# Kernel tuning notes

Measured on AMD Instinct MI355X. Metric: run time of the kernel, lower is better.

## Reference

```python
import jax, jax.numpy as jnp
import numpy as np

B, S, D, H = 4, 2048, 512, 8
EPS = 1e-5

def _layer_norm(x, gamma, beta):
    mu = jnp.mean(x, axis=-1, keepdims=True)
    var = jnp.mean(jnp.square(x - mu), axis=-1, keepdims=True)
    return (x - mu) * jax.lax.rsqrt(var + EPS) * gamma + beta

def setup_inputs() -> dict:
    key = jax.random.key(0)
    ks = jax.random.split(key, 6)
    sc = 1.0 / np.sqrt(D)
    return {
        "seq_k": jax.random.normal(ks[0], (B, S, D), jnp.float32),
        "seq_q": jax.random.normal(ks[1], (B, S, D), jnp.float32),
        "seq_v": jax.random.normal(ks[2], (B, S, D), jnp.float32),
        "W1": jax.random.normal(ks[3], (D, D), jnp.float32) * sc,
        "W2": jax.random.normal(ks[4], (D, D), jnp.float32) * sc,
        "W3": jax.random.normal(ks[5], (D, D), jnp.float32) * sc,
        "gamma": jnp.ones((D,), jnp.float32),
        "beta": jnp.zeros((D,), jnp.float32),
    }

def reference(seq_k, seq_q, seq_v, W1, W2, W3, gamma, beta):
    # is_layer_norm=True: pre-LN on values; seq_v_value is the normed v
    v_in = _layer_norm(seq_v, gamma, beta)
    # nn.Linear(bias=False): y = x @ W^T
    q = seq_q @ W1.T
    k = seq_k @ W2.T
    v = v_in @ W3.T
    hd = D // H
    q = q.reshape(B, S, H, hd).transpose(0, 2, 1, 3)  # b h s d
    k = k.reshape(B, S, H, hd).transpose(0, 2, 1, 3)
    v = v.reshape(B, S, H, hd).transpose(0, 2, 1, 3)
    # faithful quirk: scores = K @ Q^T, unscaled
    scores = jnp.einsum("bhid,bhjd->bhij", k, q)  # b h s s
    attn = jax.nn.softmax(scores, axis=-1)
    out = jnp.einsum("bhij,bhjd->bhid", attn, v)  # b h s d
    out = out.transpose(0, 2, 1, 3).reshape(B, S, D)
    out = out + v_in                 # is_residual=True
    return _layer_norm(out, gamma, beta)  # final LN
```

## Files before the change

kernel.cpp:

```cpp
#include <hip/hip_runtime.h>
#include <math.h>

#define BB 4
#define SS 2048
#define DD 512
#define HH 8
#define HD 64
#define NTOK (BB*SS)
#define EPS 1e-5f
#define NE ((size_t)NTOK * DD)
#define WN ((size_t)DD * DD)
#define LOG2E 1.4426950408889634f

typedef _Float16 half8v __attribute__((ext_vector_type(8)));
typedef _Float16 half4v __attribute__((ext_vector_type(4)));
typedef _Float16 half2v __attribute__((ext_vector_type(2)));
typedef float f32x4 __attribute__((ext_vector_type(4)));

__device__ __forceinline__ float fast_exp2(float x) {
#if __has_builtin(__builtin_amdgcn_exp2f)
    return __builtin_amdgcn_exp2f(x);
#else
    return __expf(x * 0.6931471805599453f);
#endif
}

__device__ __forceinline__ half2v pack2(float a, float b) {
    return __builtin_bit_cast(half2v, __builtin_amdgcn_cvt_pkrtz(a, b));
}

__device__ __forceinline__ half4v pack4(float a, float b, float c, float d) {
    half2v lo = pack2(a, b);
    half2v hi = pack2(c, d);
    half4v r; r[0] = lo[0]; r[1] = lo[1]; r[2] = hi[0]; r[3] = hi[1];
    return r;
}

__device__ __forceinline__ void gload_lds16(const void* g, void* l) {
    __builtin_amdgcn_global_load_lds(
        (const __attribute__((address_space(1))) unsigned int*)g,
        (__attribute__((address_space(3))) unsigned int*)l, 16, 0, 0);
}

__global__ __launch_bounds__(256) void ln_kernel(const _Float16* __restrict__ x,
                                                 const _Float16* __restrict__ res,
                                                 const float* __restrict__ gamma,
                                                 const float* __restrict__ beta,
                                                 float* __restrict__ y) {
    int row = blockIdx.x;
    int t = threadIdx.x;
    half2v xv = *(const half2v*)&x[(size_t)row * DD + 2 * t];
    half2v rv = *(const half2v*)&res[(size_t)row * DD + 2 * t];
    float2 v;
    v.x = (float)xv[0] + (float)rv[0];
    v.y = (float)xv[1] + (float)rv[1];
    float s = v.x + v.y;
    float ss = v.x * v.x + v.y * v.y;
    #pragma unroll
    for (int off = 32; off; off >>= 1) {
        s  += __shfl_down(s,  off);
        ss += __shfl_down(ss, off);
    }
    __shared__ float ws0[4], ws1[4];
    int wid = t >> 6, lane = t & 63;
    if (lane == 0) { ws0[wid] = s; ws1[wid] = ss; }
    __syncthreads();
    __shared__ float mu_s, rstd_s;
    if (t == 0) {
        float S0 = ws0[0] + ws0[1] + ws0[2] + ws0[3];
        float S1 = ws1[0] + ws1[1] + ws1[2] + ws1[3];
        float mu = S0 * (1.0f / DD);
        float var = S1 * (1.0f / DD) - mu * mu;
        mu_s = mu;
        rstd_s = rsqrtf(var + EPS);
    }
    __syncthreads();
    float mu = mu_s, rstd = rstd_s;
    float2 g = ((const float2*)gamma)[t];
    float2 bb = ((const float2*)beta)[t];
    float2 o;
    o.x = (v.x - mu) * rstd * g.x + bb.x;
    o.y = (v.y - mu) * rstd * g.y + bb.y;
    ((float2*)(y + (size_t)row * DD))[t] = o;
}

__global__ __launch_bounds__(256) void prep_kernel(const float* __restrict__ seq_v,
                                                   const float* __restrict__ seq_q,
                                                   const float* __restrict__ seq_k,
                                                   const float* __restrict__ W1,
                                                   const float* __restrict__ W2,
                                                   const float* __restrict__ W3,
                                                   const float* __restrict__ gamma,
                                                   const float* __restrict__ beta,
                                                   _Float16* __restrict__ v16,
                                                   _Float16* __restrict__ qk16,
                                                   _Float16* __restrict__ w16) {
    int bid = blockIdx.x;
    int t = threadIdx.x;
    if (bid < NTOK) {
        int row = bid;
        float2 v = ((const float2*)(seq_v + (size_t)row * DD))[t];
        float s = v.x + v.y;
        float ss = v.x * v.x + v.y * v.y;
        #pragma unroll
        for (int off = 32; off; off >>= 1) {
            s  += __shfl_down(s,  off);
            ss += __shfl_down(ss, off);
        }
        __shared__ float ws0[4], ws1[4];
        int wid = t >> 6, lane = t & 63;
        if (lane == 0) { ws0[wid] = s; ws1[wid] = ss; }
        __syncthreads();
        __shared__ float mu_s, rstd_s;
        if (t == 0) {
            float S0 = ws0[0] + ws0[1] + ws0[2] + ws0[3];
            float S1 = ws1[0] + ws1[1] + ws1[2] + ws1[3];
            float mu = S0 * (1.0f / DD);
            float var = S1 * (1.0f / DD) - mu * mu;
            mu_s = mu;
            rstd_s = rsqrtf(var + EPS);
        }
        __syncthreads();
        float mu = mu_s, rstd = rstd_s;
        float2 g = ((const float2*)gamma)[t];
        float2 bb = ((const float2*)beta)[t];
        float2 o;
        o.x = (v.x - mu) * rstd * g.x + bb.x;
        o.y = (v.y - mu) * rstd * g.y + bb.y;
        *(half2v*)&v16[(size_t)row * DD + 2 * t] = pack2(o.x, o.y);
    } else if (bid < 2 * NTOK) {
        size_t i = ((size_t)(bid - NTOK) * 256 + t) * 4;
        const float* src = (i < NE) ? (seq_q + i) : (seq_k + (i - NE));
        float4 v = *(const float4*)src;
        *(half4v*)(qk16 + i) = pack4(v.x, v.y, v.z, v.w);
    } else {
        size_t i = ((size_t)(bid - 2 * NTOK) * 256 + t) * 4;
        const float* src; float sc;
        if (i < WN)          { src = W1 + i;            sc = LOG2E; }
        else if (i < 2 * WN) { src = W2 + (i - WN);     sc = 1.0f; }
        else                 { src = W3 + (i - 2 * WN); sc = 1.0f; }
        float4 v = *(const float4*)src;
        *(half4v*)(w16 + i) = pack4(v.x * sc, v.y * sc, v.z * sc, v.w * sc);
    }
}

#define GBM 128
#define GBN 128
#define GBK 64
__global__ __launch_bounds__(256) void gemm_mfma(const _Float16* __restrict__ Aall,
                                                 const _Float16* __restrict__ Wall,
                                                 _Float16* __restrict__ Call,
                                                 _Float16* __restrict__ vtOut) {
    __shared__ __align__(16) _Float16 smem[2][2 * GBM * GBK];
    int wg = blockIdx.x;
    int local = wg >> 3;
    int z = local >> 5;
    int r5 = local & 31;
    int my = (wg & 7) * 8 + (r5 >> 2);
    int nx = r5 & 3;
    bool isv = (z == 2);
    const _Float16* A = Aall + (size_t)z * NE;
    const _Float16* W = Wall + (size_t)z * WN;
    int t = threadIdx.x, w = t >> 6, lane = t & 63, q = lane >> 4, ln = lane & 15;
    int lrow = lane >> 3, lseg = lane & 7;
    int m0 = my * GBM, n0 = nx * GBN;
    int wm = w & 1, wn = w >> 1;
    f32x4 acc[4][4];
    #pragma unroll
    for (int mt = 0; mt < 4; ++mt)
        #pragma unroll
        for (int nt = 0; nt < 4; ++nt)
            acc[mt][nt] = (f32x4){0.f, 0.f, 0.f, 0.f};

    int gs = lseg ^ lrow;

    auto stage = [&](int k0, int buf) {
        _Float16* Asb = smem[buf];
        _Float16* Wsb = smem[buf] + GBM * GBK;
        #pragma unroll
        for (int p = 0; p < 4; ++p) {
            int rr = w * 32 + p * 8 + lrow;
            gload_lds16(A + (size_t)(m0 + rr) * DD + k0 + gs * 8,
                        Asb + (size_t)(w * 32 + p * 8) * GBK);
            gload_lds16(W + (size_t)(n0 + rr) * DD + k0 + gs * 8,
                        Wsb + (size_t)(w * 32 + p * 8) * GBK);
        }
    };

    stage(0, 0);
    const int NK = DD / GBK;
    for (int ki = 0; ki < NK; ++ki) {
        int cur = ki & 1;
        __syncthreads();
        if (ki + 1 < NK) stage((ki + 1) * GBK, cur ^ 1);
        _Float16* Asb = smem[cur];
        _Float16* Wsb = smem[cur] + GBM * GBK;
        __builtin_amdgcn_s_setprio(1);
        #pragma unroll
        for (int kk = 0; kk < 2; ++kk) {
            int ch = ((4 * kk + q) ^ (ln & 7)) * 8;
            half8v af[4], wf[4];
            #pragma unroll
            for (int mt = 0; mt < 4; ++mt)
                af[mt] = *(half8v*)&Asb[(wm * 64 + mt * 16 + ln) * GBK + ch];
            #pragma unroll
            for (int nt = 0; nt < 4; ++nt)
                wf[nt] = *(half8v*)&Wsb[(wn * 64 + nt * 16 + ln) * GBK + ch];
            if (!isv) {
                #pragma unroll
                for (int mt = 0; mt < 4; ++mt)
                    #pragma unroll
                    for (int nt = 0; nt < 4; ++nt)
                        acc[mt][nt] = __builtin_amdgcn_mfma_f32_16x16x32_f16(
                            wf[nt], af[mt], acc[mt][nt], 0, 0, 0);
            } else {
                #pragma unroll
                for (int mt = 0; mt < 4; ++mt)
                    #pragma unroll
                    for (int nt = 0; nt < 4; ++nt)
                        acc[mt][nt] = __builtin_amdgcn_mfma_f32_16x16x32_f16(
                            af[mt], wf[nt], acc[mt][nt], 0, 0, 0);
            }
        }
        __builtin_amdgcn_s_setprio(0);
    }

    _Float16* esm = &smem[0][0];
    if (!isv) {
        #pragma unroll
        for (int mt = 0; mt < 4; ++mt) {
            int mloc = wm * 64 + mt * 16 + ln;
            #pragma unroll
            for (int nt = 0; nt < 4; ++nt) {
                int nloc = wn * 64 + nt * 16 + q * 4;
                int cs = (nloc >> 3) ^ (mloc & 7);
                char* p = (char*)esm + mloc * 256 + cs * 16 + (nloc & 7) * 2;
                *(half4v*)p = pack4(acc[mt][nt][0], acc[mt][nt][1],
                                    acc[mt][nt][2], acc[mt][nt][3]);
            }
        }
    } else {
        #pragma unroll
        for (int nt = 0; nt < 4; ++nt) {
            int dloc = wn * 64 + nt * 16 + ln;
            #pragma unroll
            for (int mt = 0; mt < 4; ++mt) {
                int sloc = wm * 64 + mt * 16 + q * 4;
                int cs = (sloc >> 3) ^ (dloc & 7);
                char* p = (char*)esm + dloc * 256 + cs * 16 + (sloc & 7) * 2;
                *(half4v*)p = pack4(acc[mt][nt][0], acc[mt][nt][1],
                                    acc[mt][nt][2], acc[mt][nt][3]);
            }
        }
    }
    __syncthreads();
    int bq = m0 >> 11, sbase = m0 & (SS - 1);
    if (!isv) {
        _Float16* C = Call + (size_t)z * NE;
        #pragma unroll
        for (int p = 0; p < 8; ++p) {
            int id = p * 256 + t;
            int rr = id >> 4, c = id & 15;
            half8v vv = *(half8v*)((char*)esm + rr * 256 + ((c ^ (rr & 7)) * 16));
            int n = n0 + c * 8;
            int h = n >> 6, d0 = n & 63;
            *(half8v*)&C[((size_t)(bq * HH + h) * SS + (sbase + rr)) * HD + d0] = vv;
        }
    } else {
        #pragma unroll
        for (int p = 0; p < 8; ++p) {
            int id = p * 256 + t;
            int rr = id >> 4, c = id & 15;
            half8v vv = *(half8v*)((char*)esm + rr * 256 + ((c ^ (rr & 7)) * 16));
            int d = n0 + rr;
            int h = d >> 6, dd = d & 63;
            *(half8v*)&vtOut[((size_t)(bq * HH + h) * HD + dd) * SS + sbase + c * 8] = vv;
        }
    }
}

#define AI 128
#define AJ 64
__global__ __launch_bounds__(512, 4) void attn_mfma(const _Float16* __restrict__ qh,
                                                    const _Float16* __restrict__ kh,
                                                    const _Float16* __restrict__ vt,
                                                    _Float16* __restrict__ outp) {
    __shared__ __align__(16) _Float16 Qt[2][AJ * HD];
    __shared__ __align__(16) _Float16 Vs[2][HD * AJ];
    __shared__ __align__(16) _Float16 Ps[AI * AJ];
    int t = threadIdx.x, w = t >> 6, lane = t & 63, q = lane >> 4, ln = lane & 15;
    int wg = blockIdx.x;
    int slot = wg >> 3;
    int bh = (wg & 7) * 4 + (slot >> 4);
    int i0 = (slot & 15) * AI;
    int b = bh >> 3, h = bh & 7;
    const _Float16* Kb = kh + (size_t)bh * SS * HD;
    const _Float16* Qb = qh + (size_t)bh * SS * HD;
    const _Float16* Vb = vt + (size_t)bh * HD * SS;

    half8v kf[2];
    #pragma unroll
    for (int kk = 0; kk < 2; ++kk)
        kf[kk] = *(const half8v*)&Kb[(size_t)(i0 + w * 16 + ln) * HD + kk * 32 + q * 8];

    f32x4 oacc[4], lacc;
    float m_run = -3.0e38f;
    lacc = (f32x4){0.f, 0.f, 0.f, 0.f};
    #pragma unroll
    for (int mtd = 0; mtd < 4; ++mtd) oacc[mtd] = (f32x4){0.f, 0.f, 0.f, 0.f};
    half8v ones;
    #pragma unroll
    for (int e = 0; e < 8; ++e) ones[e] = (_Float16)1.0f;
    const f32x4 zf = (f32x4){0.f, 0.f, 0.f, 0.f};

    int sr = t >> 3;
    int sc = t & 7;
    int ssw = sc ^ (sr & 7);

    gload_lds16(Qb + (size_t)sr * HD + ssw * 8, &Qt[0][(size_t)w * 512]);
    gload_lds16(Vb + (size_t)sr * SS + ssw * 8, &Vs[0][(size_t)w * 512]);

    const int NITER = SS / AJ;

#define ATTN_STEP(JT, CUR, DOPF)                                              \
    {                                                                         \
        __syncthreads();                                                      \
        if (DOPF) {                                                           \
            int j1 = ((JT) + 1) * AJ;                                         \
            gload_lds16(Qb + (size_t)(j1 + sr) * HD + ssw * 8,                \
                        &Qt[(CUR) ^ 1][(size_t)w * 512]);                     \
            gload_lds16(Vb + (size_t)sr * SS + j1 + ssw * 8,                  \
                        &Vs[(CUR) ^ 1][(size_t)w * 512]);                     \
        }                                                                     \
        f32x4 sacc[4];                                                        \
        __builtin_amdgcn_s_setprio(1);                                        \
        _Pragma("unroll")                                                     \
        for (int mt = 0; mt < 4; ++mt) {                                      \
            half8v qf = *(half8v*)&Qt[CUR][(mt * 16 + ln) * HD +              \
                                           (q ^ (ln & 7)) * 8];               \
            sacc[mt] = __builtin_amdgcn_mfma_f32_16x16x32_f16(                \
                qf, kf[0], zf, 0, 0, 0);                                      \
        }                                                                     \
        _Pragma("unroll")                                                     \
        for (int mt = 0; mt < 4; ++mt) {                                      \
            half8v qf = *(half8v*)&Qt[CUR][(mt * 16 + ln) * HD +              \
                                           ((4 + q) ^ (ln & 7)) * 8];         \
            sacc[mt] = __builtin_amdgcn_mfma_f32_16x16x32_f16(                \
                qf, kf[1], sacc[mt], 0, 0, 0);                                \
        }                                                                     \
        __builtin_amdgcn_s_setprio(0);                                        \
        float mx = fmaxf(fmaxf(sacc[0][0], sacc[0][1]),                       \
                         fmaxf(sacc[0][2], sacc[0][3]));                      \
        _Pragma("unroll")                                                     \
        for (int mt = 1; mt < 4; ++mt) {                                      \
            float m2 = fmaxf(fmaxf(sacc[mt][0], sacc[mt][1]),                 \
                             fmaxf(sacc[mt][2], sacc[mt][3]));                \
            mx = fmaxf(mx, m2);                                               \
        }                                                                     \
        mx = fmaxf(mx, __shfl_xor(mx, 16));                                   \
        mx = fmaxf(mx, __shfl_xor(mx, 32));                                   \
        if (__any(mx > m_run + 7.0f)) {                                       \
            float mn = fmaxf(m_run, mx);                                      \
            float a = fast_exp2(m_run - mn);                                  \
            lacc *= a;                                                        \
            _Pragma("unroll")                                                 \
            for (int mtd = 0; mtd < 4; ++mtd) oacc[mtd] *= a;                 \
            m_run = mn;                                                       \
        }                                                                     \
        int rp = w * 16 + ln;                                                 \
        _Pragma("unroll")                                                     \
        for (int mt = 0; mt < 4; ++mt) {                                      \
            float p0 = fast_exp2(sacc[mt][0] - m_run);                        \
            float p1 = fast_exp2(sacc[mt][1] - m_run);                        \
            float p2 = fast_exp2(sacc[mt][2] - m_run);                        \
            float p3 = fast_exp2(sacc[mt][3] - m_run);                        \
            int cw = mt * 2 + (q >> 1);                                       \
            int pos = cw ^ (ln & 7);                                          \
            *(half4v*)&Ps[(size_t)rp * AJ + pos * 8 + (q & 1) * 4] =          \
                pack4(p0, p1, p2, p3);                                        \
        }                                                                     \
        __builtin_amdgcn_s_setprio(1);                                        \
        _Pragma("unroll")                                                     \
        for (int ks = 0; ks < 2; ++ks) {                                      \
            int pos = ((ks * 4 + q) ^ (ln & 7)) * 8;                          \
            half8v pf = *(half8v*)&Ps[(size_t)(w * 16 + ln) * AJ + pos];      \
            lacc = __builtin_amdgcn_mfma_f32_16x16x32_f16(                    \
                ones, pf, lacc, 0, 0, 0);                                     \
            _Pragma("unroll")                                                 \
            for (int mtd = 0; mtd < 4; ++mtd) {                               \
                half8v vf = *(half8v*)&Vs[CUR][(size_t)(mtd * 16 + ln) * AJ + \
                                               pos];                          \
                oacc[mtd] = __builtin_amdgcn_mfma_f32_16x16x32_f16(           \
                    vf, pf, oacc[mtd], 0, 0, 0);                              \
            }                                                                 \
        }                                                                     \
        __builtin_amdgcn_s_setprio(0);                                        \
    }

    for (int jtp = 0; jtp < NITER / 2; ++jtp) {
        int jt0 = 2 * jtp;
        ATTN_STEP(jt0, 0, true);
        ATTN_STEP(jt0 + 1, 1, (jtp + 1 < NITER / 2));
    }
#undef ATTN_STEP

    float inv = 1.0f / lacc[0];
    int i = i0 + w * 16 + ln;
    #pragma unroll
    for (int mtd = 0; mtd < 4; ++mtd) {
        half4v o = pack4(oacc[mtd][0] * inv, oacc[mtd][1] * inv,
                         oacc[mtd][2] * inv, oacc[mtd][3] * inv);
        *(half4v*)&outp[(size_t)(b * SS + i) * DD + h * HD + mtd * 16 + q * 4] = o;
    }
}

extern "C" void kernel_launch(void* const* d_in, const int* in_sizes, int n_in,
                              void* d_out, int out_size, void* d_ws, size_t ws_size,
                              hipStream_t stream) {
    const float* seq_k = (const float*)d_in[0];
    const float* seq_q = (const float*)d_in[1];
    const float* seq_v = (const float*)d_in[2];
    const float* W1    = (const float*)d_in[3];
    const float* W2    = (const float*)d_in[4];
    const float* W3    = (const float*)d_in[5];
    const float* gamma = (const float*)d_in[6];
    const float* beta  = (const float*)d_in[7];
    float* out = (float*)d_out;

    const size_t MB = 1024 * 1024;
    char* w8 = (char*)d_ws;
    _Float16* ao   = (_Float16*)w8;
    _Float16* a16  = (_Float16*)(w8 + 16 * MB);
    _Float16* w16  = (_Float16*)(w8 + 40 * MB);
    _Float16* qh   = (_Float16*)(w8 + 48 * MB);
    _Float16* vt   = (_Float16*)(w8 + 64 * MB);

    _Float16* q16 = a16;
    _Float16* v16 = a16 + 2 * NE;
    _Float16* kh  = qh + NE;

    hipLaunchKernelGGL(prep_kernel, dim3(2 * NTOK + 768), dim3(256), 0, stream,
                       seq_v, seq_q, seq_k, W1, W2, W3, gamma, beta,
                       v16, q16, w16);
    hipLaunchKernelGGL(gemm_mfma, dim3((DD / GBN) * (NTOK / GBM) * 3), dim3(256), 0, stream,
                       a16, w16, qh, vt);
    hipLaunchKernelGGL(attn_mfma, dim3((SS / AI) * BB * HH), dim3(512), 0, stream,
                       qh, kh, vt, ao);
    hipLaunchKernelGGL(ln_kernel, dim3(NTOK), dim3(256), 0, stream,
                       ao, v16, gamma, beta, out);
}
```

Baseline: 184.3 us.

## Replace LDS round-trip for P tile with permlane register swaps

The attention kernel no longer writes the softmax probabilities to a shared-memory Ps buffer and reads them back as MFMA B-operands. It now packs them to fp16 in registers and redistributes them across lanes with permlane32/permlane16 swap operations. The row-max reduction also uses permlane swaps instead of shfl_xor. This removes LDS traffic and a shared buffer, which may allow better occupancy. The cost is extra VALU selects and permute instructions, and correctness depends on the lane mapping matching the MFMA operand layout.

```diff
diff --git a/kernel.cpp b/kernel.cpp
--- a/kernel.cpp
+++ b/kernel.cpp
@@ -16,6 +16,8 @@
 typedef _Float16 half4v __attribute__((ext_vector_type(4)));
 typedef _Float16 half2v __attribute__((ext_vector_type(2)));
 typedef float f32x4 __attribute__((ext_vector_type(4)));
+typedef unsigned int u32x2 __attribute__((ext_vector_type(2)));
+typedef unsigned int u32x4 __attribute__((ext_vector_type(4)));
 
 __device__ __forceinline__ float fast_exp2(float x) {
 #if __has_builtin(__builtin_amdgcn_exp2f)
@@ -34,6 +36,39 @@
     half2v hi = pack2(c, d);
     half4v r; r[0] = lo[0]; r[1] = lo[1]; r[2] = hi[0]; r[3] = hi[1];
     return r;
+}
+
+__device__ __forceinline__ unsigned pk2u(float a, float b) {
+    return __builtin_bit_cast(unsigned, __builtin_amdgcn_cvt_pkrtz(a, b));
+}
+
+__device__ __forceinline__ u32x2 p16sw(unsigned x, unsigned y) {
+#if __has_builtin(__builtin_amdgcn_permlane16_swap)
+    return __builtin_amdgcn_permlane16_swap(x, y, false, false);
+#else
+    int odd = (__lane_id() >> 4) & 1;
+    u32x2 r;
+    r[0] = odd ? __shfl_xor((int)y, 16) : (int)x;
+    r[1] = odd ? (int)y : __shfl_xor((int)x, 16);
+    return r;
+#endif
+}
+__device__ __forceinline__ u32x2 p32sw(unsigned x, unsigned y) {
+#if __has_builtin(__builtin_amdgcn_permlane32_swap)
+    return __builtin_amdgcn_permlane32_swap(x, y, false, false);
+#else
+    int hi = (__lane_id() >> 5) & 1;
+    u32x2 r;
+    r[0] = hi ? __shfl_xor((int)y, 32) : (int)x;
+    r[1] = hi ? (int)y : __shfl_xor((int)x, 32);
+    return r;
+#endif
+}
+__device__ __forceinline__ float fbits(unsigned u) {
+    return __builtin_bit_cast(float, u);
+}
+__device__ __forceinline__ unsigned ubits(float f) {
+    return __builtin_bit_cast(unsigned, f);
 }
 
 __device__ __forceinline__ void gload_lds16(const void* g, void* l) {
@@ -287,8 +322,8 @@
                                                     _Float16* __restrict__ outp) {
     __shared__ __align__(16) _Float16 Qt[2][AJ * HD];
     __shared__ __align__(16) _Float16 Vs[2][HD * AJ];
-    __shared__ __align__(16) _Float16 Ps[AI * AJ];
     int t = threadIdx.x, w = t >> 6, lane = t & 63, q = lane >> 4, ln = lane & 15;
+    bool oddq = (q & 1) != 0;
     int wg = blockIdx.x;
     int slot = wg >> 3;
     int bh = (wg & 7) * 4 + (slot >> 4);
@@ -357,8 +392,12 @@
                              fmaxf(sacc[mt][2], sacc[mt][3]));                \
             mx = fmaxf(mx, m2);                                               \
         }                                                                     \
-        mx = fmaxf(mx, __shfl_xor(mx, 16));                                   \
-        mx = fmaxf(mx, __shfl_xor(mx, 32));                                   \
+        {                   \
+            u32x2 mA = p16sw(ubits(mx), ubits(mx));                           \
+            mx = fmaxf(mx, fmaxf(fbits(mA[0]), fbits(mA[1])));                \
+            u32x2 mB = p32sw(ubits(mx), ubits(mx));                           \
+            mx = fmaxf(mx, fmaxf(fbits(mB[0]), fbits(mB[1])));                \
+        }                                                                     \
         if (__any(mx > m_run + 7.0f)) {                                       \
             float mn = fmaxf(m_run, mx);                                      \
             float a = fast_exp2(m_run - mn);                                  \
@@ -367,23 +406,32 @@
             for (int mtd = 0; mtd < 4; ++mtd) oacc[mtd] *= a;                 \
             m_run = mn;                                                       \
         }                                                                     \
-        int rp = w * 16 + ln;                                                 \
+        unsigned pk[4][2];                                                    \
         _Pragma("unroll")                                                     \
         for (int mt = 0; mt < 4; ++mt) {                                      \
             float p0 = fast_exp2(sacc[mt][0] - m_run);                        \
             float p1 = fast_exp2(sacc[mt][1] - m_run);                        \
             float p2 = fast_exp2(sacc[mt][2] - m_run);                        \
             float p3 = fast_exp2(sacc[mt][3] - m_run);                        \
-            int cw = mt * 2 + (q >> 1);                                       \
-            int pos = cw ^ (ln & 7);                                          \
-            *(half4v*)&Ps[(size_t)rp * AJ + pos * 8 + (q & 1) * 4] =          \
-                pack4(p0, p1, p2, p3);                                        \
+            pk[mt][0] = pk2u(p0, p1);                                         \
+            pk[mt][1] = pk2u(p2, p3);                                         \
         }                                                                     \
         __builtin_amdgcn_s_setprio(1);                                        \
         _Pragma("unroll")                                                     \
         for (int ks = 0; ks < 2; ++ks) {                                      \
+            u32x2 s0p = p32sw(pk[2 * ks][0], pk[2 * ks + 1][0]);              \
+            u32x2 s1p = p32sw(pk[2 * ks][1], pk[2 * ks + 1][1]);              \
+            u32x2 t0p = p16sw(s0p[1], s0p[1]);                                \
+            u32x2 u0p = p16sw(s0p[0], s0p[0]);                                \
+            u32x2 t1p = p16sw(s1p[1], s1p[1]);                                \
+            u32x2 u1p = p16sw(s1p[0], s1p[0]);                                \
+            u32x4 F;                                                          \
+            F[0] = oddq ? t0p[0] : s0p[0];                                    \
+            F[1] = oddq ? t1p[0] : s1p[0];                                    \
+            F[2] = oddq ? s0p[1] : u0p[1];                                    \
+            F[3] = oddq ? s1p[1] : u1p[1];                                    \
+            half8v pf = __builtin_bit_cast(half8v, F);                        \
             int pos = ((ks * 4 + q) ^ (ln & 7)) * 8;                          \
-            half8v pf = *(half8v*)&Ps[(size_t)(w * 16 + ln) * AJ + pos];      \
             lacc = __builtin_amdgcn_mfma_f32_16x16x32_f16(                    \
                 ones, pf, lacc, 0, 0, 0);                                     \
             _Pragma("unroll")                                                 \
```

After: 185.7 us. Within noise of the previous version (+0.7%).

## Fuse fp32-to-fp16 conversion of Q/K inputs into the projection GEMM

Applied to the files above, without the earlier changes.

Removes the separate fp16 conversion pass over seq_q and seq_k in the prep kernel. The GEMM now loads fp32 rows into registers, converts them, and writes fp16 into shared memory during the software pipeline. This saves a full write and read of two fp16 activation tensors, but GEMM blocks now read fp32 (twice the bytes) once per N-tile. They also use register staging instead of direct global-to-LDS loads, which raises register pressure.

```diff
diff --git a/kernel.cpp b/kernel.cpp
--- a/kernel.cpp
+++ b/kernel.cpp
@@ -85,15 +85,12 @@
 }
 
 __global__ __launch_bounds__(256) void prep_kernel(const float* __restrict__ seq_v,
-                                                   const float* __restrict__ seq_q,
-                                                   const float* __restrict__ seq_k,
                                                    const float* __restrict__ W1,
                                                    const float* __restrict__ W2,
                                                    const float* __restrict__ W3,
                                                    const float* __restrict__ gamma,
                                                    const float* __restrict__ beta,
                                                    _Float16* __restrict__ v16,
-                                                   _Float16* __restrict__ qk16,
                                                    _Float16* __restrict__ w16) {
     int bid = blockIdx.x;
     int t = threadIdx.x;
@@ -128,13 +125,8 @@
         o.x = (v.x - mu) * rstd * g.x + bb.x;
         o.y = (v.y - mu) * rstd * g.y + bb.y;
         *(half2v*)&v16[(size_t)row * DD + 2 * t] = pack2(o.x, o.y);
-    } else if (bid < 2 * NTOK) {
+    } else {
         size_t i = ((size_t)(bid - NTOK) * 256 + t) * 4;
-        const float* src = (i < NE) ? (seq_q + i) : (seq_k + (i - NE));
-        float4 v = *(const float4*)src;
-        *(half4v*)(qk16 + i) = pack4(v.x, v.y, v.z, v.w);
-    } else {
-        size_t i = ((size_t)(bid - 2 * NTOK) * 256 + t) * 4;
         const float* src; float sc;
         if (i < WN)          { src = W1 + i;            sc = LOG2E; }
         else if (i < 2 * WN) { src = W2 + (i - WN);     sc = 1.0f; }
@@ -147,8 +139,10 @@
 #define GBM 128
 #define GBN 128
 #define GBK 64
-__global__ __launch_bounds__(256) void gemm_mfma(const _Float16* __restrict__ Aall,
-                                                 const _Float16* __restrict__ Wall,
+__global__ __launch_bounds__(256) void gemm_mfma(const float* __restrict__ Qf32,
+                                                 const float* __restrict__ Kf32,
+                                                 const _Float16* __restrict__ v16,
+                                                 const _Float16* __restrict__ w16,
                                                  _Float16* __restrict__ Call,
                                                  _Float16* __restrict__ vtOut) {
     __shared__ __align__(16) _Float16 smem[2][2 * GBM * GBK];
@@ -159,8 +153,8 @@
     int my = (wg & 7) * 8 + (r5 >> 2);
     int nx = r5 & 3;
     bool isv = (z == 2);
-    const _Float16* A = Aall + (size_t)z * NE;
-    const _Float16* W = Wall + (size_t)z * WN;
+    const float* Af = (z == 0) ? Qf32 : Kf32;
+    const _Float16* W = w16 + (size_t)z * WN;
     int t = threadIdx.x, w = t >> 6, lane = t & 63, q = lane >> 4, ln = lane & 15;
     int lrow = lane >> 3, lseg = lane & 7;
     int m0 = my * GBM, n0 = nx * GBN;
@@ -174,25 +168,67 @@
 
     int gs = lseg ^ lrow;
 
-    auto stage = [&](int k0, int buf) {
-        _Float16* Asb = smem[buf];
+    auto stageW = [&](int k0, int buf) {
         _Float16* Wsb = smem[buf] + GBM * GBK;
         #pragma unroll
         for (int p = 0; p < 4; ++p) {
             int rr = w * 32 + p * 8 + lrow;
-            gload_lds16(A + (size_t)(m0 + rr) * DD + k0 + gs * 8,
-                        Asb + (size_t)(w * 32 + p * 8) * GBK);
             gload_lds16(W + (size_t)(n0 + rr) * DD + k0 + gs * 8,
                         Wsb + (size_t)(w * 32 + p * 8) * GBK);
         }
     };
-
-    stage(0, 0);
+    auto stageAv = [&](int k0, int buf) {
+        _Float16* Asb = smem[buf];
+        #pragma unroll
+        for (int p = 0; p < 4; ++p) {
+            int rr = w * 32 + p * 8 + lrow;
+            gload_lds16(v16 + (size_t)(m0 + rr) * DD + k0 + gs * 8,
+                        Asb + (size_t)(w * 32 + p * 8) * GBK);
+        }
+    };
+    float4 va[4][2];
+    auto loadAf32 = [&](int k0) {
+        #pragma unroll
+        for (int p = 0; p < 4; ++p) {
+            int rr = w * 32 + p * 8 + lrow;
+            const float* src = Af + (size_t)(m0 + rr) * DD + k0 + gs * 8;
+            va[p][0] = *(const float4*)src;
+            va[p][1] = *(const float4*)(src + 4);
+        }
+    };
+    auto writeAf16 = [&](int buf) {
+        _Float16* Asb = smem[buf];
+        #pragma unroll
+        for (int p = 0; p < 4; ++p) {
+            int rr = w * 32 + p * 8 + lrow;
+            half8v h8;
+            half4v lo = pack4(va[p][0].x, va[p][0].y, va[p][0].z, va[p][0].w);
+            half4v hi = pack4(va[p][1].x, va[p][1].y, va[p][1].z, va[p][1].w);
+            h8[0] = lo[0]; h8[1] = lo[1]; h8[2] = lo[2]; h8[3] = lo[3];
+            h8[4] = hi[0]; h8[5] = hi[1]; h8[6] = hi[2]; h8[7] = hi[3];
+            *(half8v*)&Asb[(size_t)rr * GBK + lseg * 8] = h8;
+        }
+    };
+
+    if (isv) {
+        stageAv(0, 0);
+    } else {
+        loadAf32(0);
+        writeAf16(0);
+    }
+    stageW(0, 0);
+
     const int NK = DD / GBK;
     for (int ki = 0; ki < NK; ++ki) {
         int cur = ki & 1;
         __syncthreads();
-        if (ki + 1 < NK) stage((ki + 1) * GBK, cur ^ 1);
+        bool pf = (ki + 1 < NK);
+        int k1 = (ki + 1) * GBK;
+        if (pf) {
+            stageW(k1, cur ^ 1);
+            if (isv) stageAv(k1, cur ^ 1);
+            else     loadAf32(k1);
+        }
         _Float16* Asb = smem[cur];
         _Float16* Wsb = smem[cur] + GBM * GBK;
         __builtin_amdgcn_s_setprio(1);
@@ -223,9 +259,11 @@
             }
         }
         __builtin_amdgcn_s_setprio(0);
+        if (pf && !isv) writeAf16(cur ^ 1);
     }
 
     _Float16* esm = &smem[0][0];
+    __syncthreads();
     if (!isv) {
         #pragma unroll
         for (int mt = 0; mt < 4; ++mt) {
@@ -430,20 +468,16 @@
     const size_t MB = 1024 * 1024;
     char* w8 = (char*)d_ws;
     _Float16* ao   = (_Float16*)w8;
-    _Float16* a16  = (_Float16*)(w8 + 16 * MB);
+    _Float16* v16  = (_Float16*)(w8 + 32 * MB);
     _Float16* w16  = (_Float16*)(w8 + 40 * MB);
     _Float16* qh   = (_Float16*)(w8 + 48 * MB);
     _Float16* vt   = (_Float16*)(w8 + 64 * MB);
-
-    _Float16* q16 = a16;
-    _Float16* v16 = a16 + 2 * NE;
-    _Float16* kh  = qh + NE;
-
-    hipLaunchKernelGGL(prep_kernel, dim3(2 * NTOK + 768), dim3(256), 0, stream,
-                       seq_v, seq_q, seq_k, W1, W2, W3, gamma, beta,
-                       v16, q16, w16);
+    _Float16* kh   = qh + NE;
+
+    hipLaunchKernelGGL(prep_kernel, dim3(NTOK + 768), dim3(256), 0, stream,
+                       seq_v, W1, W2, W3, gamma, beta, v16, w16);
     hipLaunchKernelGGL(gemm_mfma, dim3((DD / GBN) * (NTOK / GBM) * 3), dim3(256), 0, stream,
-                       a16, w16, qh, vt);
+                       seq_q, seq_k, v16, w16, qh, vt);
     hipLaunchKernelGGL(attn_mfma, dim3((SS / AI) * BB * HH), dim3(512), 0, stream,
                        qh, kh, vt, ao);
     hipLaunchKernelGGL(ln_kernel, dim3(NTOK), dim3(256), 0, stream,
```

New measurement: 193.0 us. 1.05x slower.
